# Optimization experiments

Hardware: AMD Instinct MI355X
Metric: run time of the kernel (lower is better)

## Reference

```python
import jax, jax.numpy as jnp
import numpy as np

B = 8
N_SRC = 2048   # coarse points per cloud
N_DST = 8192   # dense (skip) points per cloud
C_SRC = 128
C_SKIP = 64
K = 3
BN_EPS = 1e-5
LRELU_SLOPE = 0.01


def setup_inputs() -> dict:
    key = jax.random.key(0)
    ks = jax.random.split(key, 12)
    x = jax.random.normal(ks[0], (B * N_SRC, C_SRC), dtype=jnp.float32)
    pos = jax.random.normal(ks[1], (B * N_SRC, 3), dtype=jnp.float32)
    x_skip = jax.random.normal(ks[2], (B * N_DST, C_SKIP), dtype=jnp.float32)
    pos_skip = jax.random.normal(ks[3], (B * N_DST, 3), dtype=jnp.float32)
    batch = jnp.repeat(jnp.arange(B, dtype=jnp.int64), N_SRC)
    batch_skip = jnp.repeat(jnp.arange(B, dtype=jnp.int64), N_DST)
    c_in = C_SRC + C_SKIP  # 192
    c_h = 128
    # Linear weights: torch layout [out, in]
    W1 = jax.random.normal(ks[4], (c_h, c_in), dtype=jnp.float32) / np.sqrt(c_in)
    b1 = jax.random.normal(ks[5], (c_h,), dtype=jnp.float32) * 0.01
    g1 = jnp.ones((c_h,), dtype=jnp.float32)
    be1 = jnp.zeros((c_h,), dtype=jnp.float32)
    W2 = jax.random.normal(ks[6], (c_h, c_h), dtype=jnp.float32) / np.sqrt(c_h)
    b2 = jax.random.normal(ks[7], (c_h,), dtype=jnp.float32) * 0.01
    g2 = jnp.ones((c_h,), dtype=jnp.float32)
    be2 = jnp.zeros((c_h,), dtype=jnp.float32)
    return {"x": x, "pos": pos, "batch": batch, "x_skip": x_skip,
            "pos_skip": pos_skip, "batch_skip": batch_skip,
            "W1": W1, "b1": b1, "g1": g1, "be1": be1,
            "W2": W2, "b2": b2, "g2": g2, "be2": be2}


def _knn_interpolate(x, pos, pos_skip):
    # Uniform-sized batches -> reshape and process per cloud.
    xs = x.reshape(B, N_SRC, -1)          # [B, Ns, C]
    ps = pos.reshape(B, N_SRC, 3)
    pd = pos_skip.reshape(B, N_DST, 3)
    # Squared pairwise distances per cloud: [B, Nd, Ns]
    d2 = jnp.sum((pd[:, :, None, :] - ps[:, None, :, :]) ** 2, axis=-1)
    neg_d2, idx = jax.lax.top_k(-d2, K)   # k nearest -> [B, Nd, K]
    w = 1.0 / jnp.maximum(-neg_d2, 1e-16)  # inverse squared distance weights
    feats = jax.vmap(lambda f, i: f[i])(xs, idx)  # [B, Nd, K, C]
    y = jnp.sum(w[..., None] * feats, axis=2) / jnp.sum(w, axis=2, keepdims=True)
    return y.reshape(B * N_DST, -1)


def _mlp_block(h, W, b, g, be):
    h = h @ W.T + b
    h = jnp.where(h > 0, h, LRELU_SLOPE * h)  # LeakyReLU
    mean = jnp.mean(h, axis=0)
    var = jnp.mean((h - mean) ** 2, axis=0)   # biased var (BN training mode)
    h = (h - mean) * jax.lax.rsqrt(var + BN_EPS)
    return h * g + be


def reference(x, pos, batch, x_skip, pos_skip, batch_skip,
              W1, b1, g1, be1, W2, b2, g2, be2):
    h = _knn_interpolate(x, pos, pos_skip)      # [B*Nd, C_SRC]
    h = jnp.concatenate([h, x_skip], axis=1)    # [B*Nd, C_SRC+C_SKIP]
    h = _mlp_block(h, W1, b1, g1, be1)
    h = _mlp_block(h, W2, b2, g2, be2)
    return (h, pos_skip, batch_skip)
```

## Files before the change

kernel.cpp:

```cpp
#include <hip/hip_runtime.h>
#include <math.h>

#define NB 8
#define N_SRC 2048
#define N_DST 8192
#define C_SRC 128
#define C_SKIP 64
#define C_IN 192
#define C_H 128
#define N_ROWS (NB * N_DST)
#define BN_EPS 1e-5f
#define SLOPE 0.01f
#define GEMM_BLOCKS (N_ROWS / 64)

using short8 = __attribute__((ext_vector_type(8))) short;
using f32x4  = __attribute__((ext_vector_type(4))) float;
using sf16   = __attribute__((ext_vector_type(16))) float;

static __device__ __forceinline__ unsigned short f2bf(float f) {
    unsigned u = __builtin_bit_cast(unsigned, f);
    u = u + 0x7FFFu + ((u >> 16) & 1u);
    return (unsigned short)(u >> 16);
}

__global__ __launch_bounds__(256) void k_prep(const float* __restrict__ W1,
                                              unsigned short* __restrict__ W1bf,
                                              const float* __restrict__ W2,
                                              unsigned short* __restrict__ W2bf,
                                              const float* __restrict__ pos,
                                              float4* __restrict__ pos4,
                                              const float* __restrict__ pos_skip,
                                              const int* __restrict__ batch_skip,
                                              float* __restrict__ out_pos,
                                              float* __restrict__ out_batch) {
    int gid = blockIdx.x * 256 + threadIdx.x;
    int stride = gridDim.x * 256;
    for (int i = gid; i < C_H * C_IN; i += stride) W1bf[i] = f2bf(W1[i]);
    for (int i = gid; i < C_H * C_H; i += stride)  W2bf[i] = f2bf(W2[i]);
    for (int p = gid; p < NB * N_SRC; p += stride) {
        pos4[p] = make_float4(pos[p * 3 + 0], pos[p * 3 + 1], pos[p * 3 + 2], 0.f);
    }
    for (int i = gid; i < N_ROWS * 3 / 4; i += stride) {
        ((float4*)out_pos)[i] = ((const float4*)pos_skip)[i];
    }
    for (int i = gid; i < N_ROWS; i += stride) {
        out_batch[i] = (float)batch_skip[i];
    }
}

__global__ __launch_bounds__(512, 8) void k_fused1(
    const float4* __restrict__ pos4, const float* __restrict__ pos_skip,
    const float* __restrict__ x, const float* __restrict__ x_skip,
    const unsigned short* __restrict__ Wbf, const float* __restrict__ bias,
    float* __restrict__ out, float* __restrict__ ps, float* __restrict__ pq) {
    __shared__ __align__(16) unsigned short Ash[64][200];
    __shared__ float sS[4][128];
    __shared__ float sQ[4][128];
    __shared__ int   midx[64][3];
    __shared__ float mw[64][3];

    float* cd = (float*)&Ash[0][0];
    int*   ci = (int*)((char*)&Ash[0][0] + 6144);

    int tid = threadIdx.x;
    int l = tid & 63;
    int v = __builtin_amdgcn_readfirstlane(tid >> 6);
    int cloud = blockIdx.x >> 7;
    int r0 = blockIdx.x * 64;

    int dst = r0 + l;
    float px = pos_skip[dst * 3 + 0];
    float py = pos_skip[dst * 3 + 1];
    float pz = pos_skip[dst * 3 + 2];

    float rr0 = 3.4e38f, rr1 = 3.4e38f, rr2 = 3.4e38f;
    int   ii0 = 0, ii1 = 0, ii2 = 0;

    const char* sp = (const char*)(pos4 + (cloud << 11) + (v << 8));
    for (int g = 0; g < 32; ++g) {
        sf16 A, B;
        asm volatile("s_load_dwordx16 %0, %2, 0x0\n\t"
                     "s_load_dwordx16 %1, %2, 0x40\n\t"
                     "s_waitcnt lgkmcnt(0)"
                     : "=s"(A), "=s"(B)
                     : "s"(sp));
        sp += 128;
        int jb = (v << 8) + g * 8;
#pragma unroll
        for (int k = 0; k < 4; ++k) {
            float dx = px - A[4 * k], dy = py - A[4 * k + 1], dz = pz - A[4 * k + 2];
            float d = fmaf(dx, dx, fmaf(dy, dy, dz * dz));
            if (d < rr2) {
                int jj = jb + k;
                bool c0 = d < rr0, c1 = d < rr1;
                ii2 = c1 ? ii1 : jj;              rr2 = c1 ? rr1 : d;
                ii1 = c1 ? (c0 ? ii0 : jj) : ii1; rr1 = c1 ? (c0 ? rr0 : d) : rr1;
                ii0 = c0 ? jj : ii0;              rr0 = c0 ? d : rr0;
            }
        }
#pragma unroll
        for (int k = 0; k < 4; ++k) {
            float dx = px - B[4 * k], dy = py - B[4 * k + 1], dz = pz - B[4 * k + 2];
            float d = fmaf(dx, dx, fmaf(dy, dy, dz * dz));
            if (d < rr2) {
                int jj = jb + 4 + k;
                bool c0 = d < rr0, c1 = d < rr1;
                ii2 = c1 ? ii1 : jj;              rr2 = c1 ? rr1 : d;
                ii1 = c1 ? (c0 ? ii0 : jj) : ii1; rr1 = c1 ? (c0 ? rr0 : d) : rr1;
                ii0 = c0 ? jj : ii0;              rr0 = c0 ? d : rr0;
            }
        }
    }
    cd[(v * 64 + l) * 3 + 0] = rr0; ci[(v * 64 + l) * 3 + 0] = ii0;
    cd[(v * 64 + l) * 3 + 1] = rr1; ci[(v * 64 + l) * 3 + 1] = ii1;
    cd[(v * 64 + l) * 3 + 2] = rr2; ci[(v * 64 + l) * 3 + 2] = ii2;
    __syncthreads();

    if (tid < 64) {
        float e0 = 3.4e38f, e1 = 3.4e38f, e2 = 3.4e38f;
        int   m0 = 0, m1 = 0, m2 = 0;
#pragma unroll
        for (int s = 0; s < 8; ++s) {
#pragma unroll
            for (int t = 0; t < 3; ++t) {
                float d = cd[(s * 64 + tid) * 3 + t];
                int  jj = ci[(s * 64 + tid) * 3 + t];
                if (d < e2) {
                    bool c0 = d < e0, c1 = d < e1;
                    m2 = c1 ? m1 : jj;            e2 = c1 ? e1 : d;
                    m1 = c1 ? (c0 ? m0 : jj) : m1; e1 = c1 ? (c0 ? e0 : d) : e1;
                    m0 = c0 ? jj : m0;            e0 = c0 ? d : e0;
                }
            }
        }
        float w0 = 1.f / fmaxf(e0, 1e-16f);
        float w1 = 1.f / fmaxf(e1, 1e-16f);
        float w2 = 1.f / fmaxf(e2, 1e-16f);
        float inv = 1.f / (w0 + w1 + w2);
        midx[tid][0] = m0; midx[tid][1] = m1; midx[tid][2] = m2;
        mw[tid][0] = w0 * inv; mw[tid][1] = w1 * inv; mw[tid][2] = w2 * inv;
    }
    __syncthreads();

    const float* xb = x + (size_t)cloud * N_SRC * C_SRC;
    for (int rr = v * 8; rr < v * 8 + 8; ++rr) {
        int j0 = midx[rr][0], j1 = midx[rr][1], j2 = midx[rr][2];
        float w0 = mw[rr][0], w1 = mw[rr][1], w2 = mw[rr][2];
        const float2* x0v = (const float2*)(xb + (size_t)j0 * C_SRC);
        const float2* x1v = (const float2*)(xb + (size_t)j1 * C_SRC);
        const float2* x2v = (const float2*)(xb + (size_t)j2 * C_SRC);
        float2 a = x0v[l], b = x1v[l], c = x2v[l];
        float v0 = w0 * a.x + w1 * b.x + w2 * c.x;
        float v1 = w0 * a.y + w1 * b.y + w2 * c.y;
        ((unsigned*)&Ash[rr][0])[l] = (unsigned)f2bf(v0) | ((unsigned)f2bf(v1) << 16);
        Ash[rr][128 + l] = f2bf(x_skip[(size_t)(r0 + rr) * C_SKIP + l]);
    }
    __syncthreads();

    if (v < 4) {
        int w = v;
        int cl = l & 15, kh = l >> 4;
        f32x4 acc[8];
#pragma unroll
        for (int n = 0; n < 8; ++n) {
            float bv = bias[n * 16 + cl];
            acc[n][0] = bv; acc[n][1] = bv; acc[n][2] = bv; acc[n][3] = bv;
        }
        const unsigned short* wb = Wbf + (size_t)cl * C_IN + kh * 8;
        for (int kt = 0; kt < 6; ++kt) {
            short8 af = *(const short8*)&Ash[w * 16 + cl][kt * 32 + kh * 8];
#pragma unroll
            for (int n = 0; n < 8; ++n) {
                short8 bf = *(const short8*)(wb + (size_t)n * 16 * C_IN + kt * 32);
                acc[n] = __builtin_amdgcn_mfma_f32_16x16x32_bf16(af, bf, acc[n], 0, 0, 0);
            }
        }

#pragma unroll
        for (int n = 0; n < 8; ++n) {
            float s = 0.f, q = 0.f;
            int col = n * 16 + cl;
#pragma unroll
            for (int j = 0; j < 4; ++j) {
                int row = r0 + w * 16 + kh * 4 + j;
                float z = acc[n][j];
                z = z > 0.f ? z : SLOPE * z;
                out[(size_t)row * C_H + col] = z;
                s += z; q += z * z;
            }
            s += __shfl_xor(s, 16); s += __shfl_xor(s, 32);
            q += __shfl_xor(q, 16); q += __shfl_xor(q, 32);
            if (l < 16) {
                sS[w][n * 16 + l] = s;
                sQ[w][n * 16 + l] = q;
            }
        }
    }
    __syncthreads();
    if (tid < 128) {
        float s = sS[0][tid] + sS[1][tid] + sS[2][tid] + sS[3][tid];
        float q = sQ[0][tid] + sQ[1][tid] + sQ[2][tid] + sQ[3][tid];
        ps[blockIdx.x * C_H + tid] = s;
        pq[blockIdx.x * C_H + tid] = q;
    }
}

__global__ __launch_bounds__(256) void k_reduce(const float* __restrict__ ps,
                                                const float* __restrict__ pq,
                                                const float* __restrict__ g,
                                                const float* __restrict__ be,
                                                float* __restrict__ a_out,
                                                float* __restrict__ c_out) {
    int col = blockIdx.x;
    float s = 0.f, q = 0.f;
    for (int b = threadIdx.x; b < GEMM_BLOCKS; b += 256) {
        s += ps[b * C_H + col];
        q += pq[b * C_H + col];
    }
    for (int off = 32; off; off >>= 1) {
        s += __shfl_down(s, off);
        q += __shfl_down(q, off);
    }
    __shared__ float rs[4], rq[4];
    if ((threadIdx.x & 63) == 0) { rs[threadIdx.x >> 6] = s; rq[threadIdx.x >> 6] = q; }
    __syncthreads();
    if (threadIdx.x == 0) {
        s = rs[0] + rs[1] + rs[2] + rs[3];
        q = rq[0] + rq[1] + rq[2] + rq[3];
        float mean = s / (float)N_ROWS;
        float var  = q / (float)N_ROWS - mean * mean;
        float a = g[col] * rsqrtf(var + BN_EPS);
        a_out[col] = a;
        c_out[col] = be[col] - mean * a;
    }
}

__global__ __launch_bounds__(256) void k_g2a(const float* __restrict__ h,
                                             const unsigned short* __restrict__ Wbf,
                                             const float* __restrict__ b2,
                                             const float* __restrict__ a1,
                                             const float* __restrict__ c1,
                                             float* __restrict__ ps,
                                             float* __restrict__ pq,
                                             unsigned short* __restrict__ z2bf) {
    __shared__ __align__(16) unsigned short Ash[64][136];
    __shared__ float sS[4][128];
    __shared__ float sQ[4][128];

    int r0 = blockIdx.x * 64;
    int tid = threadIdx.x;
    int l = tid & 63, w = tid >> 6;

    const float* src = h + (size_t)r0 * C_H;
    for (int i = tid * 4; i < 64 * C_H; i += 1024) {
        float4 v = *(const float4*)&src[i];
        int r = i >> 7, c = i & 127;
        float4 av = *(const float4*)&a1[c];
        float4 cv = *(const float4*)&c1[c];
        unsigned lo = (unsigned)f2bf(fmaf(av.x, v.x, cv.x)) |
                      ((unsigned)f2bf(fmaf(av.y, v.y, cv.y)) << 16);
        unsigned hi = (unsigned)f2bf(fmaf(av.z, v.z, cv.z)) |
                      ((unsigned)f2bf(fmaf(av.w, v.w, cv.w)) << 16);
        *(uint2*)&Ash[r][c] = make_uint2(lo, hi);
    }
    __syncthreads();

    int cl = l & 15, kh = l >> 4;
    f32x4 acc[8];
#pragma unroll
    for (int n = 0; n < 8; ++n) {
        float bv = b2[n * 16 + cl];
        acc[n][0] = bv; acc[n][1] = bv; acc[n][2] = bv; acc[n][3] = bv;
    }
    const unsigned short* wb = Wbf + (size_t)cl * C_H + kh * 8;
    for (int kt = 0; kt < 4; ++kt) {
        short8 af = *(const short8*)&Ash[w * 16 + cl][kt * 32 + kh * 8];
#pragma unroll
        for (int n = 0; n < 8; ++n) {
            short8 bf = *(const short8*)(wb + (size_t)n * 16 * C_H + kt * 32);
            acc[n] = __builtin_amdgcn_mfma_f32_16x16x32_bf16(af, bf, acc[n], 0, 0, 0);
        }
    }

    float pss[8], pqs[8];
#pragma unroll
    for (int n = 0; n < 8; ++n) {
        float s = 0.f, q = 0.f;
#pragma unroll
        for (int j = 0; j < 4; ++j) {
            float z = acc[n][j];
            z = z > 0.f ? z : SLOPE * z;
            acc[n][j] = z;
            s += z; q += z * z;
        }
        s += __shfl_xor(s, 16); s += __shfl_xor(s, 32);
        q += __shfl_xor(q, 16); q += __shfl_xor(q, 32);
        pss[n] = s; pqs[n] = q;
    }

    if (z2bf) {
        __syncthreads();
        unsigned short* Az = (unsigned short*)&Ash[0][0];
#pragma unroll
        for (int n = 0; n < 8; ++n) {
            int col = n * 16 + cl;
#pragma unroll
            for (int j = 0; j < 4; ++j) {
                Az[(w * 16 + kh * 4 + j) * 128 + col] = f2bf(acc[n][j]);
            }
        }
    }
    if (l < 16) {
#pragma unroll
        for (int n = 0; n < 8; ++n) {
            sS[w][n * 16 + l] = pss[n];
            sQ[w][n * 16 + l] = pqs[n];
        }
    }
    __syncthreads();
    if (z2bf) {
        const uint4* Asrc = (const uint4*)&Ash[0][0];
        uint4* zdst = (uint4*)(z2bf + (size_t)r0 * C_H);
        for (int i = tid; i < 64 * C_H / 8; i += 256) zdst[i] = Asrc[i];
    }
    if (tid < 128) {
        float s = sS[0][tid] + sS[1][tid] + sS[2][tid] + sS[3][tid];
        float q = sQ[0][tid] + sQ[1][tid] + sQ[2][tid] + sQ[3][tid];
        ps[blockIdx.x * C_H + tid] = s;
        pq[blockIdx.x * C_H + tid] = q;
    }
}

__global__ __launch_bounds__(256) void k_final(const unsigned short* __restrict__ z2bf,
                                               const float* __restrict__ a2,
                                               const float* __restrict__ c2,
                                               float* __restrict__ out_h) {
    __shared__ float sa[128], sc[128];
    int tid = threadIdx.x;
    if (tid < 128) { sa[tid] = a2[tid]; sc[tid] = c2[tid]; }
    __syncthreads();

    int gid = blockIdx.x * 256 + tid;
    int stride = gridDim.x * 256;
    const uint4* zsrc = (const uint4*)z2bf;
    for (int i = gid; i < N_ROWS * C_H / 8; i += stride) {
        uint4 v = zsrc[i];
        int c0 = (i * 8) & 127;
        float4 o0, o1;
        o0.x = fmaf(sa[c0 + 0], __builtin_bit_cast(float, (v.x & 0xFFFFu) << 16), sc[c0 + 0]);
        o0.y = fmaf(sa[c0 + 1], __builtin_bit_cast(float, (v.x & 0xFFFF0000u)), sc[c0 + 1]);
        o0.z = fmaf(sa[c0 + 2], __builtin_bit_cast(float, (v.y & 0xFFFFu) << 16), sc[c0 + 2]);
        o0.w = fmaf(sa[c0 + 3], __builtin_bit_cast(float, (v.y & 0xFFFF0000u)), sc[c0 + 3]);
        o1.x = fmaf(sa[c0 + 4], __builtin_bit_cast(float, (v.z & 0xFFFFu) << 16), sc[c0 + 4]);
        o1.y = fmaf(sa[c0 + 5], __builtin_bit_cast(float, (v.z & 0xFFFF0000u)), sc[c0 + 5]);
        o1.z = fmaf(sa[c0 + 6], __builtin_bit_cast(float, (v.w & 0xFFFFu) << 16), sc[c0 + 6]);
        o1.w = fmaf(sa[c0 + 7], __builtin_bit_cast(float, (v.w & 0xFFFF0000u)), sc[c0 + 7]);
        *(float4*)&out_h[(size_t)i * 8]     = o0;
        *(float4*)&out_h[(size_t)i * 8 + 4] = o1;
    }
}

__global__ __launch_bounds__(256) void k_g2b(float* __restrict__ h,
                                             const unsigned short* __restrict__ Wbf,
                                             const float* __restrict__ b2,
                                             const float* __restrict__ a1,
                                             const float* __restrict__ c1,
                                             const float* __restrict__ a2,
                                             const float* __restrict__ c2) {
    __shared__ __align__(16) unsigned short Ash[64][136];

    int r0 = blockIdx.x * 64;
    int tid = threadIdx.x;
    int l = tid & 63, w = tid >> 6;

    const float* src = h + (size_t)r0 * C_H;
    for (int i = tid * 4; i < 64 * C_H; i += 1024) {
        float4 v = *(const float4*)&src[i];
        int r = i >> 7, c = i & 127;
        float4 av = *(const float4*)&a1[c];
        float4 cv = *(const float4*)&c1[c];
        unsigned lo = (unsigned)f2bf(fmaf(av.x, v.x, cv.x)) |
                      ((unsigned)f2bf(fmaf(av.y, v.y, cv.y)) << 16);
        unsigned hi = (unsigned)f2bf(fmaf(av.z, v.z, cv.z)) |
                      ((unsigned)f2bf(fmaf(av.w, v.w, cv.w)) << 16);
        *(uint2*)&Ash[r][c] = make_uint2(lo, hi);
    }
    __syncthreads();

    int cl = l & 15, kh = l >> 4;
    f32x4 acc[8];
#pragma unroll
    for (int n = 0; n < 8; ++n) {
        float bv = b2[n * 16 + cl];
        acc[n][0] = bv; acc[n][1] = bv; acc[n][2] = bv; acc[n][3] = bv;
    }
    const unsigned short* wb = Wbf + (size_t)cl * C_H + kh * 8;
    for (int kt = 0; kt < 4; ++kt) {
        short8 af = *(const short8*)&Ash[w * 16 + cl][kt * 32 + kh * 8];
#pragma unroll
        for (int n = 0; n < 8; ++n) {
            short8 bf = *(const short8*)(wb + (size_t)n * 16 * C_H + kt * 32);
            acc[n] = __builtin_amdgcn_mfma_f32_16x16x32_bf16(af, bf, acc[n], 0, 0, 0);
        }
    }

#pragma unroll
    for (int n = 0; n < 8; ++n) {
        int col = n * 16 + cl;
        float av = a2[col], cv = c2[col];
#pragma unroll
        for (int j = 0; j < 4; ++j) {
            int row = r0 + w * 16 + kh * 4 + j;
            float z = acc[n][j];
            z = z > 0.f ? z : SLOPE * z;
            h[(size_t)row * C_H + col] = av * z + cv;
        }
    }
}

extern "C" void kernel_launch(void* const* d_in, const int* in_sizes, int n_in,
                              void* d_out, int out_size, void* d_ws, size_t ws_size,
                              hipStream_t stream) {
    const float* x          = (const float*)d_in[0];
    const float* pos        = (const float*)d_in[1];
    const float* x_skip     = (const float*)d_in[3];
    const float* pos_skip   = (const float*)d_in[4];
    const int*   batch_skip = (const int*)d_in[5];
    const float* W1  = (const float*)d_in[6];
    const float* b1  = (const float*)d_in[7];
    const float* g1  = (const float*)d_in[8];
    const float* be1 = (const float*)d_in[9];
    const float* W2  = (const float*)d_in[10];
    const float* b2  = (const float*)d_in[11];
    const float* g2  = (const float*)d_in[12];
    const float* be2 = (const float*)d_in[13];

    float* out_h     = (float*)d_out;
    float* out_pos   = out_h + (size_t)N_ROWS * C_H;
    float* out_batch = out_pos + (size_t)N_ROWS * 3;

    float* wsf = (float*)d_ws;
    float4* pos4         = (float4*)wsf;
    unsigned short* W1bf = (unsigned short*)(wsf + 65536);
    unsigned short* W2bf = (unsigned short*)(wsf + 77824);
    float* p1s = wsf + 86016;
    float* p1q = p1s + 131072;
    float* p2s = p1q + 131072;
    float* p2q = p2s + 131072;
    float* a1g = p2q + 131072;
    float* c1g = a1g + 128;
    float* a2g = c1g + 128;
    float* c2g = a2g + 128;
    unsigned short* z2bf = (unsigned short*)(c2g + 128);
    size_t ws_needed = ((size_t)(610816) * 4) + (size_t)N_ROWS * C_H * 2;
    bool use_z = ws_size >= ws_needed;

    k_prep<<<256, 256, 0, stream>>>(W1, W1bf, W2, W2bf, pos, pos4,
                                    pos_skip, batch_skip, out_pos, out_batch);
    k_fused1<<<GEMM_BLOCKS, 512, 0, stream>>>(pos4, pos_skip, x, x_skip, W1bf, b1,
                                              out_h, p1s, p1q);
    k_reduce<<<C_H, 256, 0, stream>>>(p1s, p1q, g1, be1, a1g, c1g);
    k_g2a<<<GEMM_BLOCKS, 256, 0, stream>>>(out_h, W2bf, b2, a1g, c1g, p2s, p2q,
                                           use_z ? z2bf : (unsigned short*)nullptr);
    k_reduce<<<C_H, 256, 0, stream>>>(p2s, p2q, g2, be2, a2g, c2g);
    if (use_z) {
        k_final<<<1024, 256, 0, stream>>>(z2bf, a2g, c2g, out_h);
    } else {
        k_g2b<<<GEMM_BLOCKS, 256, 0, stream>>>(out_h, W2bf, b2, a1g, c1g, a2g, c2g);
    }
}
```

Before: 124.4 us.

## Store layer-1 activations as bf16, split GEMM1 over all waves, interleave cloud tiles

The first layer now writes its LeakyReLU output as bf16 into a workspace buffer, staged through shared memory for coalesced stores. The second-layer GEMM reads that buffer in place of the fp32 output and reuses it in place for z2, which halves the intermediate traffic. GEMM1 now runs on all 8 waves (4 row groups by 2 column halves) instead of 4. Block-to-tile mapping interleaves clouds so that concurrent blocks cover different clouds. Extra bf16 rounding of h1 adds a small accuracy risk, and k_g2a reads and writes the same buffer, which is safe only because each block touches its own rows.

```diff
diff --git a/kernel.cpp b/kernel.cpp
--- a/kernel.cpp
+++ b/kernel.cpp
@@ -21,6 +21,12 @@
     unsigned u = __builtin_bit_cast(unsigned, f);
     u = u + 0x7FFFu + ((u >> 16) & 1u);
     return (unsigned short)(u >> 16);
+}
+static __device__ __forceinline__ float bflo(unsigned v) {
+    return __builtin_bit_cast(float, (v & 0xFFFFu) << 16);
+}
+static __device__ __forceinline__ float bfhi(unsigned v) {
+    return __builtin_bit_cast(float, v & 0xFFFF0000u);
 }
 
 __global__ __launch_bounds__(256) void k_prep(const float* __restrict__ W1,
@@ -52,7 +58,8 @@
     const float4* __restrict__ pos4, const float* __restrict__ pos_skip,
     const float* __restrict__ x, const float* __restrict__ x_skip,
     const unsigned short* __restrict__ Wbf, const float* __restrict__ bias,
-    float* __restrict__ out, float* __restrict__ ps, float* __restrict__ pq) {
+    float* __restrict__ out, unsigned short* __restrict__ h1bf,
+    float* __restrict__ ps, float* __restrict__ pq) {
     __shared__ __align__(16) unsigned short Ash[64][200];
     __shared__ float sS[4][128];
     __shared__ float sQ[4][128];
@@ -65,8 +72,10 @@
     int tid = threadIdx.x;
     int l = tid & 63;
     int v = __builtin_amdgcn_readfirstlane(tid >> 6);
-    int cloud = blockIdx.x >> 7;
-    int r0 = blockIdx.x * 64;
+    int blk = blockIdx.x;
+    int cloud = blk & 7;
+    int tile  = blk >> 3;
+    int r0 = cloud * N_DST + tile * 64;
 
     int dst = r0 + l;
     float px = pos_skip[dst * 3 + 0];
@@ -157,51 +166,80 @@
     }
     __syncthreads();
 
-    if (v < 4) {
-        int w = v;
-        int cl = l & 15, kh = l >> 4;
-        f32x4 acc[8];
-#pragma unroll
-        for (int n = 0; n < 8; ++n) {
-            float bv = bias[n * 16 + cl];
-            acc[n][0] = bv; acc[n][1] = bv; acc[n][2] = bv; acc[n][3] = bv;
-        }
-        const unsigned short* wb = Wbf + (size_t)cl * C_IN + kh * 8;
-        for (int kt = 0; kt < 6; ++kt) {
-            short8 af = *(const short8*)&Ash[w * 16 + cl][kt * 32 + kh * 8];
-#pragma unroll
-            for (int n = 0; n < 8; ++n) {
-                short8 bf = *(const short8*)(wb + (size_t)n * 16 * C_IN + kt * 32);
-                acc[n] = __builtin_amdgcn_mfma_f32_16x16x32_bf16(af, bf, acc[n], 0, 0, 0);
+    int wr = v & 3, wc = v >> 2;
+    int cl = l & 15, kh = l >> 4;
+    f32x4 acc[4];
+#pragma unroll
+    for (int n = 0; n < 4; ++n) {
+        float bv = bias[wc * 64 + n * 16 + cl];
+        acc[n][0] = bv; acc[n][1] = bv; acc[n][2] = bv; acc[n][3] = bv;
+    }
+    const unsigned short* wb = Wbf + (size_t)(wc * 4) * 16 * C_IN +
+                               (size_t)cl * C_IN + kh * 8;
+    for (int kt = 0; kt < 6; ++kt) {
+        short8 af = *(const short8*)&Ash[wr * 16 + cl][kt * 32 + kh * 8];
+#pragma unroll
+        for (int n = 0; n < 4; ++n) {
+            short8 bf = *(const short8*)(wb + (size_t)n * 16 * C_IN + kt * 32);
+            acc[n] = __builtin_amdgcn_mfma_f32_16x16x32_bf16(af, bf, acc[n], 0, 0, 0);
+        }
+    }
+
+    float pss[4], pqs[4];
+#pragma unroll
+    for (int n = 0; n < 4; ++n) {
+        float s = 0.f, q = 0.f;
+#pragma unroll
+        for (int j = 0; j < 4; ++j) {
+            float z = acc[n][j];
+            z = z > 0.f ? z : SLOPE * z;
+            acc[n][j] = z;
+            s += z; q += z * z;
+        }
+        s += __shfl_xor(s, 16); s += __shfl_xor(s, 32);
+        q += __shfl_xor(q, 16); q += __shfl_xor(q, 32);
+        pss[n] = s; pqs[n] = q;
+    }
+
+    __syncthreads();
+    if (l < 16) {
+#pragma unroll
+        for (int n = 0; n < 4; ++n) {
+            sS[wr][wc * 64 + n * 16 + l] = pss[n];
+            sQ[wr][wc * 64 + n * 16 + l] = pqs[n];
+        }
+    }
+    if (h1bf) {
+        unsigned short* Az = (unsigned short*)&Ash[0][0];
+#pragma unroll
+        for (int n = 0; n < 4; ++n) {
+            int col = wc * 64 + n * 16 + cl;
+#pragma unroll
+            for (int j = 0; j < 4; ++j) {
+                Az[(wr * 16 + kh * 4 + j) * 128 + col] = f2bf(acc[n][j]);
             }
         }
-
-#pragma unroll
-        for (int n = 0; n < 8; ++n) {
-            float s = 0.f, q = 0.f;
-            int col = n * 16 + cl;
+    } else {
+#pragma unroll
+        for (int n = 0; n < 4; ++n) {
+            int col = wc * 64 + n * 16 + cl;
 #pragma unroll
             for (int j = 0; j < 4; ++j) {
-                int row = r0 + w * 16 + kh * 4 + j;
-                float z = acc[n][j];
-                z = z > 0.f ? z : SLOPE * z;
-                out[(size_t)row * C_H + col] = z;
-                s += z; q += z * z;
+                out[(size_t)(r0 + wr * 16 + kh * 4 + j) * C_H + col] = acc[n][j];
             }
-            s += __shfl_xor(s, 16); s += __shfl_xor(s, 32);
-            q += __shfl_xor(q, 16); q += __shfl_xor(q, 32);
-            if (l < 16) {
-                sS[w][n * 16 + l] = s;
-                sQ[w][n * 16 + l] = q;
-            }
-        }
-    }
-    __syncthreads();
+        }
+    }
+    __syncthreads();
+    if (h1bf) {
+        const uint4* Asrc = (const uint4*)&Ash[0][0];
+        uint4* zdst = (uint4*)(h1bf + (size_t)r0 * C_H);
+        for (int i = tid; i < 64 * C_H / 8; i += 512) zdst[i] = Asrc[i];
+    }
     if (tid < 128) {
         float s = sS[0][tid] + sS[1][tid] + sS[2][tid] + sS[3][tid];
         float q = sQ[0][tid] + sQ[1][tid] + sQ[2][tid] + sQ[3][tid];
-        ps[blockIdx.x * C_H + tid] = s;
-        pq[blockIdx.x * C_H + tid] = q;
+        ps[blk * C_H + tid] = s;
+        pq[blk * C_H + tid] = q;
     }
 }
 
@@ -236,13 +274,13 @@
 }
 
 __global__ __launch_bounds__(256) void k_g2a(const float* __restrict__ h,
+                                             unsigned short* __restrict__ h1bf,
                                              const unsigned short* __restrict__ Wbf,
                                              const float* __restrict__ b2,
                                              const float* __restrict__ a1,
                                              const float* __restrict__ c1,
                                              float* __restrict__ ps,
-                                             float* __restrict__ pq,
-                                             unsigned short* __restrict__ z2bf) {
+                                             float* __restrict__ pq) {
     __shared__ __align__(16) unsigned short Ash[64][136];
     __shared__ float sS[4][128];
     __shared__ float sQ[4][128];
@@ -251,17 +289,38 @@
     int tid = threadIdx.x;
     int l = tid & 63, w = tid >> 6;
 
-    const float* src = h + (size_t)r0 * C_H;
-    for (int i = tid * 4; i < 64 * C_H; i += 1024) {
-        float4 v = *(const float4*)&src[i];
-        int r = i >> 7, c = i & 127;
-        float4 av = *(const float4*)&a1[c];
-        float4 cv = *(const float4*)&c1[c];
-        unsigned lo = (unsigned)f2bf(fmaf(av.x, v.x, cv.x)) |
-                      ((unsigned)f2bf(fmaf(av.y, v.y, cv.y)) << 16);
-        unsigned hi = (unsigned)f2bf(fmaf(av.z, v.z, cv.z)) |
-                      ((unsigned)f2bf(fmaf(av.w, v.w, cv.w)) << 16);
-        *(uint2*)&Ash[r][c] = make_uint2(lo, hi);
+    if (h1bf) {
+        const uint4* src = (const uint4*)(h1bf + (size_t)r0 * C_H);
+        for (int i = tid; i < 64 * C_H / 8; i += 256) {
+            uint4 vv = src[i];
+            int c0 = (i * 8) & 127, r = (i * 8) >> 7;
+            float4 a0 = *(const float4*)&a1[c0];
+            float4 a4 = *(const float4*)&a1[c0 + 4];
+            float4 c0v = *(const float4*)&c1[c0];
+            float4 c4v = *(const float4*)&c1[c0 + 4];
+            unsigned o0 = (unsigned)f2bf(fmaf(a0.x, bflo(vv.x), c0v.x)) |
+                          ((unsigned)f2bf(fmaf(a0.y, bfhi(vv.x), c0v.y)) << 16);
+            unsigned o1 = (unsigned)f2bf(fmaf(a0.z, bflo(vv.y), c0v.z)) |
+                          ((unsigned)f2bf(fmaf(a0.w, bfhi(vv.y), c0v.w)) << 16);
+            unsigned o2 = (unsigned)f2bf(fmaf(a4.x, bflo(vv.z), c4v.x)) |
+                          ((unsigned)f2bf(fmaf(a4.y, bfhi(vv.z), c4v.y)) << 16);
+            unsigned o3 = (unsigned)f2bf(fmaf(a4.z, bflo(vv.w), c4v.z)) |
+                          ((unsigned)f2bf(fmaf(a4.w, bfhi(vv.w), c4v.w)) << 16);
+            *(uint4*)&Ash[r][c0] = make_uint4(o0, o1, o2, o3);
+        }
+    } else {
+        const float* src = h + (size_t)r0 * C_H;
+        for (int i = tid * 4; i < 64 * C_H; i += 1024) {
+            float4 vf = *(const float4*)&src[i];
+            int r = i >> 7, c = i & 127;
+            float4 av = *(const float4*)&a1[c];
+            float4 cv = *(const float4*)&c1[c];
+            unsigned lo = (unsigned)f2bf(fmaf(av.x, vf.x, cv.x)) |
+                          ((unsigned)f2bf(fmaf(av.y, vf.y, cv.y)) << 16);
+            unsigned hi = (unsigned)f2bf(fmaf(av.z, vf.z, cv.z)) |
+                          ((unsigned)f2bf(fmaf(av.w, vf.w, cv.w)) << 16);
+            *(uint2*)&Ash[r][c] = make_uint2(lo, hi);
+        }
     }
     __syncthreads();
 
@@ -298,7 +357,7 @@
         pss[n] = s; pqs[n] = q;
     }
 
-    if (z2bf) {
+    if (h1bf) {
         __syncthreads();
         unsigned short* Az = (unsigned short*)&Ash[0][0];
 #pragma unroll
@@ -318,9 +377,9 @@
         }
     }
     __syncthreads();
-    if (z2bf) {
+    if (h1bf) {
         const uint4* Asrc = (const uint4*)&Ash[0][0];
-        uint4* zdst = (uint4*)(z2bf + (size_t)r0 * C_H);
+        uint4* zdst = (uint4*)(h1bf + (size_t)r0 * C_H);
         for (int i = tid; i < 64 * C_H / 8; i += 256) zdst[i] = Asrc[i];
     }
     if (tid < 128) {
@@ -347,14 +406,14 @@
         uint4 v = zsrc[i];
         int c0 = (i * 8) & 127;
         float4 o0, o1;
-        o0.x = fmaf(sa[c0 + 0], __builtin_bit_cast(float, (v.x & 0xFFFFu) << 16), sc[c0 + 0]);
-        o0.y = fmaf(sa[c0 + 1], __builtin_bit_cast(float, (v.x & 0xFFFF0000u)), sc[c0 + 1]);
-        o0.z = fmaf(sa[c0 + 2], __builtin_bit_cast(float, (v.y & 0xFFFFu) << 16), sc[c0 + 2]);
-        o0.w = fmaf(sa[c0 + 3], __builtin_bit_cast(float, (v.y & 0xFFFF0000u)), sc[c0 + 3]);
-        o1.x = fmaf(sa[c0 + 4], __builtin_bit_cast(float, (v.z & 0xFFFFu) << 16), sc[c0 + 4]);
-        o1.y = fmaf(sa[c0 + 5], __builtin_bit_cast(float, (v.z & 0xFFFF0000u)), sc[c0 + 5]);
-        o1.z = fmaf(sa[c0 + 6], __builtin_bit_cast(float, (v.w & 0xFFFFu) << 16), sc[c0 + 6]);
-        o1.w = fmaf(sa[c0 + 7], __builtin_bit_cast(float, (v.w & 0xFFFF0000u)), sc[c0 + 7]);
+        o0.x = fmaf(sa[c0 + 0], bflo(v.x), sc[c0 + 0]);
+        o0.y = fmaf(sa[c0 + 1], bfhi(v.x), sc[c0 + 1]);
+        o0.z = fmaf(sa[c0 + 2], bflo(v.y), sc[c0 + 2]);
+        o0.w = fmaf(sa[c0 + 3], bfhi(v.y), sc[c0 + 3]);
+        o1.x = fmaf(sa[c0 + 4], bflo(v.z), sc[c0 + 4]);
+        o1.y = fmaf(sa[c0 + 5], bfhi(v.z), sc[c0 + 5]);
+        o1.z = fmaf(sa[c0 + 6], bflo(v.w), sc[c0 + 6]);
+        o1.w = fmaf(sa[c0 + 7], bfhi(v.w), sc[c0 + 7]);
         *(float4*)&out_h[(size_t)i * 8]     = o0;
         *(float4*)&out_h[(size_t)i * 8 + 4] = o1;
     }
@@ -375,14 +434,14 @@
 
     const float* src = h + (size_t)r0 * C_H;
     for (int i = tid * 4; i < 64 * C_H; i += 1024) {
-        float4 v = *(const float4*)&src[i];
+        float4 vf = *(const float4*)&src[i];
         int r = i >> 7, c = i & 127;
         float4 av = *(const float4*)&a1[c];
         float4 cv = *(const float4*)&c1[c];
-        unsigned lo = (unsigned)f2bf(fmaf(av.x, v.x, cv.x)) |
-                      ((unsigned)f2bf(fmaf(av.y, v.y, cv.y)) << 16);
-        unsigned hi = (unsigned)f2bf(fmaf(av.z, v.z, cv.z)) |
-                      ((unsigned)f2bf(fmaf(av.w, v.w, cv.w)) << 16);
+        unsigned lo = (unsigned)f2bf(fmaf(av.x, vf.x, cv.x)) |
+                      ((unsigned)f2bf(fmaf(av.y, vf.y, cv.y)) << 16);
+        unsigned hi = (unsigned)f2bf(fmaf(av.z, vf.z, cv.z)) |
+                      ((unsigned)f2bf(fmaf(av.w, vf.w, cv.w)) << 16);
         *(uint2*)&Ash[r][c] = make_uint2(lo, hi);
     }
     __syncthreads();
@@ -451,20 +510,21 @@
     float* c1g = a1g + 128;
     float* a2g = c1g + 128;
     float* c2g = a2g + 128;
-    unsigned short* z2bf = (unsigned short*)(c2g + 128);
-    size_t ws_needed = ((size_t)(610816) * 4) + (size_t)N_ROWS * C_H * 2;
+    unsigned short* zbuf = (unsigned short*)(c2g + 128);
+    size_t ws_needed = ((size_t)610816 * 4) + (size_t)N_ROWS * C_H * 2;
     bool use_z = ws_size >= ws_needed;
+    unsigned short* h1bf = use_z ? zbuf : (unsigned short*)nullptr;
 
     k_prep<<<256, 256, 0, stream>>>(W1, W1bf, W2, W2bf, pos, pos4,
                                     pos_skip, batch_skip, out_pos, out_batch);
     k_fused1<<<GEMM_BLOCKS, 512, 0, stream>>>(pos4, pos_skip, x, x_skip, W1bf, b1,
-                                              out_h, p1s, p1q);
+                                              out_h, h1bf, p1s, p1q);
     k_reduce<<<C_H, 256, 0, stream>>>(p1s, p1q, g1, be1, a1g, c1g);
-    k_g2a<<<GEMM_BLOCKS, 256, 0, stream>>>(out_h, W2bf, b2, a1g, c1g, p2s, p2q,
-                                           use_z ? z2bf : (unsigned short*)nullptr);
+    k_g2a<<<GEMM_BLOCKS, 256, 0, stream>>>(out_h, h1bf, W2bf, b2, a1g, c1g,
+                                           p2s, p2q);
     k_reduce<<<C_H, 256, 0, stream>>>(p2s, p2q, g2, be2, a2g, c2g);
     if (use_z) {
-        k_final<<<1024, 256, 0, stream>>>(z2bf, a2g, c2g, out_h);
+        k_final<<<1024, 256, 0, stream>>>(zbuf, a2g, c2g, out_h);
     } else {
         k_g2b<<<GEMM_BLOCKS, 256, 0, stream>>>(out_h, W2bf, b2, a1g, c1g, a2g, c2g);
     }
```

After: 112.9 us. -9.3%, faster.
